# Optimization experiments

Hardware: AMD Instinct MI355X
Metric: run time of the kernel (lower is better)

## Reference

```python
import jax, jax.numpy as jnp
import numpy as np

EPS = 1e-12  # torch F.normalize eps

def l2norm(x, axis=-1):
    n = jnp.linalg.norm(x, axis=axis, keepdims=True)
    return x / jnp.maximum(n, EPS)

def setup_inputs() -> dict:
    key = jax.random.key(0)
    ks = jax.random.split(key, 8)
    n_vocab, d, n_asp = 100000, 256, 14
    B, L, M = 512, 100, 10
    pos = jax.random.randint(ks[0], (B, L), 0, n_vocab)
    negs = jax.random.randint(ks[1], (B, M, L), 0, n_vocab)
    E_w = jax.random.normal(ks[2], (n_vocab, d), dtype=jnp.float32) * 0.1
    T_w = jax.random.normal(ks[3], (n_asp, d), dtype=jnp.float32) * 0.1
    M_w = jax.random.uniform(ks[4], (d, d), dtype=jnp.float32, minval=-0.1, maxval=0.1)
    M_b = jnp.zeros((d,), dtype=jnp.float32)
    lin_w = jax.random.normal(ks[5], (n_asp, d), dtype=jnp.float32) * 0.05
    lin_b = jnp.zeros((n_asp,), dtype=jnp.float32)
    return {"pos": pos, "negs": negs, "E_w": E_w, "T_w": T_w,
            "M_w": M_w, "M_b": M_b, "lin_w": lin_w, "lin_b": lin_b}

def reference(pos, negs, E_w, T_w, M_w, M_b, lin_w, lin_b):
    # e: [B, L, d] (original keeps e_i as [B, d, L]; layout differs, math identical)
    e = E_w[pos]
    y_s = jnp.mean(e, axis=1)                    # mean over tokens -> [B, d]
    My = y_s @ M_w.T + M_b                       # [B, d]
    d_i = jnp.tanh(jnp.einsum('bld,bd->bl', e, My))  # [B, L]
    # NOTE: original normalizes exp(d_i) by the GLOBAL sum over the whole batch
    a_i = jnp.exp(d_i) / jnp.sum(jnp.exp(d_i))   # [B, L]
    z_s = l2norm(jnp.einsum('bld,bl->bd', e, a_i))   # [B, d]
    p_t = jax.nn.softmax(z_s @ lin_w.T + lin_b, axis=1)  # [B, n_asp]
    r_s = l2norm(p_t @ T_w)                      # [B, d]
    e_n = E_w[negs]                              # [B, M, L, d]
    z_n = l2norm(jnp.mean(e_n, axis=2))          # [B, M, d]
    return (r_s, z_s, z_n)
```

## Files before the change

kernel.cpp:

```cpp
#include <hip/hip_runtime.h>
#include <math.h>

#define D 256
#define LMAX 100

__device__ __forceinline__ float wave_reduce_sum(float v) {
#pragma unroll
    for (int off = 32; off > 0; off >>= 1) v += __shfl_xor(v, off);
    return v;
}

__global__ __launch_bounds__(512) void abae_main_kernel(
    const int* __restrict__ pos, const float* __restrict__ E_w,
    const float* __restrict__ T_w, const float* __restrict__ M_w,
    const float* __restrict__ M_b, const float* __restrict__ lin_w,
    const float* __restrict__ lin_b, float* __restrict__ r_s,
    float* __restrict__ z_s, int L, int n_asp) {
    const int b    = blockIdx.x;
    const int t    = threadIdx.x;
    const int lane = t & 63;
    const int wv   = t >> 6;
    const int NW   = 8;
    const int* __restrict__ posb = pos + (size_t)b * L;

    __shared__ float  se[LMAX * D];
    __shared__ float  sy[D];
    __shared__ float  smy[D];
    __shared__ float4 sred[8][64];
    __shared__ float  slog[16];
    __shared__ float  sp[16];
    __shared__ float  sscal[8];

    const int C  = (L + NW - 1) / NW;
    const int s0 = wv * C;
    const int e0 = min(L, s0 + C);

    float4 acc = make_float4(0.f, 0.f, 0.f, 0.f);
    int l = s0;
    for (; l + 3 < e0; l += 4) {
        const int i0 = posb[l], i1 = posb[l + 1], i2 = posb[l + 2], i3 = posb[l + 3];
        const float4 a0 = ((const float4*)(E_w + (size_t)i0 * D))[lane];
        const float4 a1 = ((const float4*)(E_w + (size_t)i1 * D))[lane];
        const float4 a2 = ((const float4*)(E_w + (size_t)i2 * D))[lane];
        const float4 a3 = ((const float4*)(E_w + (size_t)i3 * D))[lane];
        ((float4*)se)[(l + 0) * 64 + lane] = a0;
        ((float4*)se)[(l + 1) * 64 + lane] = a1;
        ((float4*)se)[(l + 2) * 64 + lane] = a2;
        ((float4*)se)[(l + 3) * 64 + lane] = a3;
        acc.x += a0.x + a1.x + a2.x + a3.x;
        acc.y += a0.y + a1.y + a2.y + a3.y;
        acc.z += a0.z + a1.z + a2.z + a3.z;
        acc.w += a0.w + a1.w + a2.w + a3.w;
    }
    for (; l < e0; ++l) {
        const int idx = posb[l];
        const float4 a0 = ((const float4*)(E_w + (size_t)idx * D))[lane];
        ((float4*)se)[l * 64 + lane] = a0;
        acc.x += a0.x; acc.y += a0.y; acc.z += a0.z; acc.w += a0.w;
    }
    sred[wv][lane] = acc;
    __syncthreads();
    if (wv == 0) {
        float4 y = sred[0][lane];
#pragma unroll
        for (int w = 1; w < 8; ++w) {
            const float4 a = sred[w][lane];
            y.x += a.x; y.y += a.y; y.z += a.z; y.w += a.w;
        }
        const float invL = 1.f / (float)L;
        y.x *= invL; y.y *= invL; y.z *= invL; y.w *= invL;
        ((float4*)sy)[lane] = y;
    }
    __syncthreads();

    if (t < D) {
        float m = M_b[t];
        const float4* __restrict__ mwrow = (const float4*)(M_w + (size_t)t * D);
#pragma unroll 8
        for (int k = 0; k < D / 4; ++k) {
            const float4 v = mwrow[k];
            m += sy[4 * k + 0] * v.x + sy[4 * k + 1] * v.y +
                 sy[4 * k + 2] * v.z + sy[4 * k + 3] * v.w;
        }
        smy[t] = m;
    }
    __syncthreads();

    const float4 my4 = ((const float4*)smy)[lane];
    float4 zacc = make_float4(0.f, 0.f, 0.f, 0.f);
    l = s0;
    for (; l + 1 < e0; l += 2) {
        const float4 ea = ((const float4*)se)[(l + 0) * 64 + lane];
        const float4 eb = ((const float4*)se)[(l + 1) * 64 + lane];
        float pa = ea.x * my4.x + ea.y * my4.y + ea.z * my4.z + ea.w * my4.w;
        float pb = eb.x * my4.x + eb.y * my4.y + eb.z * my4.z + eb.w * my4.w;
#pragma unroll
        for (int off = 32; off > 0; off >>= 1) {
            pa += __shfl_xor(pa, off);
            pb += __shfl_xor(pb, off);
        }
        const float wa = expf(tanhf(pa));
        const float wb = expf(tanhf(pb));
        zacc.x += ea.x * wa + eb.x * wb;
        zacc.y += ea.y * wa + eb.y * wb;
        zacc.z += ea.z * wa + eb.z * wb;
        zacc.w += ea.w * wa + eb.w * wb;
    }
    for (; l < e0; ++l) {
        const float4 ea = ((const float4*)se)[l * 64 + lane];
        float pa = ea.x * my4.x + ea.y * my4.y + ea.z * my4.z + ea.w * my4.w;
        pa = wave_reduce_sum(pa);
        const float wa = expf(tanhf(pa));
        zacc.x += ea.x * wa; zacc.y += ea.y * wa;
        zacc.z += ea.z * wa; zacc.w += ea.w * wa;
    }
    sred[wv][lane] = zacc;
    __syncthreads();
    if (wv == 0) {
        float4 z = sred[0][lane];
#pragma unroll
        for (int w = 1; w < 8; ++w) {
            const float4 a = sred[w][lane];
            z.x += a.x; z.y += a.y; z.z += a.z; z.w += a.w;
        }
        float ss = z.x * z.x + z.y * z.y + z.z * z.z + z.w * z.w;
        ss = wave_reduce_sum(ss);
        const float inv = 1.f / fmaxf(sqrtf(ss), 1e-12f);
        z.x *= inv; z.y *= inv; z.z *= inv; z.w *= inv;
        ((float4*)(z_s + (size_t)b * D))[lane] = z;
        ((float4*)sy)[lane] = z;
    }
    __syncthreads();

    const float4 z4 = ((const float4*)sy)[lane];
    for (int a = wv; a < n_asp; a += NW) {
        const float4 w4 = ((const float4*)(lin_w + (size_t)a * D))[lane];
        float p = z4.x * w4.x + z4.y * w4.y + z4.z * w4.z + z4.w * w4.w;
        p = wave_reduce_sum(p);
        if (lane == 0) slog[a] = p + lin_b[a];
    }
    __syncthreads();
    if (t == 0) {
        float mx = -1e30f;
        for (int a = 0; a < n_asp; ++a) mx = fmaxf(mx, slog[a]);
        float s = 0.f;
        for (int a = 0; a < n_asp; ++a) {
            const float e = expf(slog[a] - mx);
            sp[a] = e; s += e;
        }
        const float invs = 1.f / s;
        for (int a = 0; a < n_asp; ++a) sp[a] *= invs;
    }
    __syncthreads();

    float r = 0.f;
    if (t < D) {
        for (int a = 0; a < n_asp; ++a) r += sp[a] * T_w[(size_t)a * D + t];
    }
    float sq = wave_reduce_sum(r * r);
    if (lane == 0) sscal[wv] = sq;
    __syncthreads();
    if (t < D) {
        const float tot = sscal[0] + sscal[1] + sscal[2] + sscal[3];
        const float inv = 1.f / fmaxf(sqrtf(tot), 1e-12f);
        r_s[(size_t)b * D + t] = r * inv;
    }
}

__global__ __launch_bounds__(256) void abae_negs_kernel(
    const int* __restrict__ negs, const float* __restrict__ E_w,
    float* __restrict__ z_n, int L) {
    const int bm   = blockIdx.x;
    const int t    = threadIdx.x;
    const int lane = t & 63;
    const int wv   = t >> 6;
    const int* __restrict__ idxp = negs + (size_t)bm * L;

    const int C  = (L + 3) / 4;
    const int s0 = wv * C;
    const int e0 = min(L, s0 + C);

    float4 acc = make_float4(0.f, 0.f, 0.f, 0.f);
    int l = s0;
    for (; l + 5 <= e0; l += 5) {
        const int i0 = idxp[l], i1 = idxp[l + 1], i2 = idxp[l + 2],
                  i3 = idxp[l + 3], i4 = idxp[l + 4];
        const float4 v0 = ((const float4*)(E_w + (size_t)i0 * D))[lane];
        const float4 v1 = ((const float4*)(E_w + (size_t)i1 * D))[lane];
        const float4 v2 = ((const float4*)(E_w + (size_t)i2 * D))[lane];
        const float4 v3 = ((const float4*)(E_w + (size_t)i3 * D))[lane];
        const float4 v4 = ((const float4*)(E_w + (size_t)i4 * D))[lane];
        acc.x += v0.x + v1.x + v2.x + v3.x + v4.x;
        acc.y += v0.y + v1.y + v2.y + v3.y + v4.y;
        acc.z += v0.z + v1.z + v2.z + v3.z + v4.z;
        acc.w += v0.w + v1.w + v2.w + v3.w + v4.w;
    }
    for (; l < e0; ++l) {
        const int idx = idxp[l];
        const float4 v = ((const float4*)(E_w + (size_t)idx * D))[lane];
        acc.x += v.x; acc.y += v.y; acc.z += v.z; acc.w += v.w;
    }

    __shared__ float4 sred[4][64];
    sred[wv][lane] = acc;
    __syncthreads();
    if (wv == 0) {
        float4 z  = sred[0][lane];
        const float4 a1 = sred[1][lane], a2 = sred[2][lane], a3 = sred[3][lane];
        const float invL = 1.f / (float)L;
        z.x = (z.x + a1.x + a2.x + a3.x) * invL;
        z.y = (z.y + a1.y + a2.y + a3.y) * invL;
        z.z = (z.z + a1.z + a2.z + a3.z) * invL;
        z.w = (z.w + a1.w + a2.w + a3.w) * invL;
        float ss = z.x * z.x + z.y * z.y + z.z * z.z + z.w * z.w;
        ss = wave_reduce_sum(ss);
        const float inv = 1.f / fmaxf(sqrtf(ss), 1e-12f);
        z.x *= inv; z.y *= inv; z.z *= inv; z.w *= inv;
        ((float4*)(z_n + (size_t)bm * D))[lane] = z;
    }
}

extern "C" void kernel_launch(void* const* d_in, const int* in_sizes, int n_in,
                              void* d_out, int out_size, void* d_ws, size_t ws_size,
                              hipStream_t stream) {
    const int*   pos   = (const int*)d_in[0];
    const int*   negs  = (const int*)d_in[1];
    const float* E_w   = (const float*)d_in[2];
    const float* T_w   = (const float*)d_in[3];
    const float* M_w   = (const float*)d_in[4];
    const float* M_b   = (const float*)d_in[5];
    const float* lin_w = (const float*)d_in[6];
    const float* lin_b = (const float*)d_in[7];
    float* out = (float*)d_out;

    const int d     = in_sizes[5];
    const int n_asp = in_sizes[7];
    const int M     = in_sizes[1] / in_sizes[0];
    const int B     = out_size / (d * (2 + M));
    const int L     = in_sizes[0] / B;
    (void)d; (void)n_in; (void)d_ws; (void)ws_size;

    float* r_s = out;
    float* z_s = out + (size_t)B * d;
    float* z_n = out + (size_t)2 * B * d;

    abae_negs_kernel<<<B * M, 256, 0, stream>>>(negs, E_w, z_n, L);
    abae_main_kernel<<<B, 512, 0, stream>>>(pos, E_w, T_w, M_w, M_b, lin_w,
                                            lin_b, r_s, z_s, L, n_asp);
}
```

Before: 253.0 us.

## Fuse pos and negs kernels into one launch; drop shared-memory embedding cache

Merges the positive-path and negative-sample kernels into a single 256-thread launch. The first B blocks do the attention path and the rest do the negative means. The 100 KB shared-memory tile of gathered embeddings is removed, and the second pass re-gathers rows from E_w (likely cache hits), which should raise occupancy and let the two workloads overlap. The M_w matvec becomes coalesced row-per-wave dot products with shuffle reductions instead of one strided row per thread. The cost is a second global gather of the positive embeddings and four waves instead of eight on the main path.

Measured after the change: 228.0 us. 1.11x faster.

```diff
diff --git a/kernel.cpp b/kernel.cpp
--- a/kernel.cpp
+++ b/kernel.cpp
@@ -2,7 +2,6 @@
 #include <math.h>
 
 #define D 256
-#define LMAX 100
 
 __device__ __forceinline__ float wave_reduce_sum(float v) {
 #pragma unroll
@@ -10,79 +9,131 @@
     return v;
 }
 
-__global__ __launch_bounds__(512) void abae_main_kernel(
-    const int* __restrict__ pos, const float* __restrict__ E_w,
-    const float* __restrict__ T_w, const float* __restrict__ M_w,
-    const float* __restrict__ M_b, const float* __restrict__ lin_w,
-    const float* __restrict__ lin_b, float* __restrict__ r_s,
-    float* __restrict__ z_s, int L, int n_asp) {
-    const int b    = blockIdx.x;
+__global__ __launch_bounds__(256) void abae_fused_kernel(
+    const int* __restrict__ pos, const int* __restrict__ negs,
+    const float* __restrict__ E_w, const float* __restrict__ T_w,
+    const float* __restrict__ M_w, const float* __restrict__ M_b,
+    const float* __restrict__ lin_w, const float* __restrict__ lin_b,
+    float* __restrict__ r_s, float* __restrict__ z_s, float* __restrict__ z_n,
+    int B, int L, int n_asp) {
     const int t    = threadIdx.x;
     const int lane = t & 63;
     const int wv   = t >> 6;
-    const int NW   = 8;
-    const int* __restrict__ posb = pos + (size_t)b * L;
-
-    __shared__ float  se[LMAX * D];
+
+    __shared__ float4 sred[4][64];
     __shared__ float  sy[D];
     __shared__ float  smy[D];
-    __shared__ float4 sred[8][64];
     __shared__ float  slog[16];
     __shared__ float  sp[16];
-    __shared__ float  sscal[8];
-
-    const int C  = (L + NW - 1) / NW;
+    __shared__ float  sscal[4];
+
+    if (blockIdx.x >= B) {
+        const int bm = blockIdx.x - B;
+        const int* __restrict__ idxp = negs + (size_t)bm * L;
+        const int C  = (L + 3) / 4;
+        const int s0 = wv * C;
+        const int e0 = min(L, s0 + C);
+
+        float4 acc = make_float4(0.f, 0.f, 0.f, 0.f);
+        int l = s0;
+        for (; l + 5 <= e0; l += 5) {
+            const int i0 = idxp[l], i1 = idxp[l + 1], i2 = idxp[l + 2],
+                      i3 = idxp[l + 3], i4 = idxp[l + 4];
+            const float4 v0 = ((const float4*)(E_w + (size_t)i0 * D))[lane];
+            const float4 v1 = ((const float4*)(E_w + (size_t)i1 * D))[lane];
+            const float4 v2 = ((const float4*)(E_w + (size_t)i2 * D))[lane];
+            const float4 v3 = ((const float4*)(E_w + (size_t)i3 * D))[lane];
+            const float4 v4 = ((const float4*)(E_w + (size_t)i4 * D))[lane];
+            acc.x += v0.x + v1.x + v2.x + v3.x + v4.x;
+            acc.y += v0.y + v1.y + v2.y + v3.y + v4.y;
+            acc.z += v0.z + v1.z + v2.z + v3.z + v4.z;
+            acc.w += v0.w + v1.w + v2.w + v3.w + v4.w;
+        }
+        for (; l < e0; ++l) {
+            const float4 v = ((const float4*)(E_w + (size_t)idxp[l] * D))[lane];
+            acc.x += v.x; acc.y += v.y; acc.z += v.z; acc.w += v.w;
+        }
+        sred[wv][lane] = acc;
+        __syncthreads();
+        if (wv == 0) {
+            float4 z  = sred[0][lane];
+            const float4 a1 = sred[1][lane], a2 = sred[2][lane], a3 = sred[3][lane];
+            const float invL = 1.f / (float)L;
+            z.x = (z.x + a1.x + a2.x + a3.x) * invL;
+            z.y = (z.y + a1.y + a2.y + a3.y) * invL;
+            z.z = (z.z + a1.z + a2.z + a3.z) * invL;
+            z.w = (z.w + a1.w + a2.w + a3.w) * invL;
+            float ss = z.x * z.x + z.y * z.y + z.z * z.z + z.w * z.w;
+            ss = wave_reduce_sum(ss);
+            const float inv = 1.f / fmaxf(sqrtf(ss), 1e-12f);
+            z.x *= inv; z.y *= inv; z.z *= inv; z.w *= inv;
+            ((float4*)(z_n + (size_t)bm * D))[lane] = z;
+        }
+        return;
+    }
+
+    const int b = blockIdx.x;
+    const int* __restrict__ posb = pos + (size_t)b * L;
+    const int C  = (L + 3) / 4;
     const int s0 = wv * C;
     const int e0 = min(L, s0 + C);
 
     float4 acc = make_float4(0.f, 0.f, 0.f, 0.f);
     int l = s0;
-    for (; l + 3 < e0; l += 4) {
+    for (; l + 4 <= e0; l += 4) {
         const int i0 = posb[l], i1 = posb[l + 1], i2 = posb[l + 2], i3 = posb[l + 3];
-        const float4 a0 = ((const float4*)(E_w + (size_t)i0 * D))[lane];
-        const float4 a1 = ((const float4*)(E_w + (size_t)i1 * D))[lane];
-        const float4 a2 = ((const float4*)(E_w + (size_t)i2 * D))[lane];
-        const float4 a3 = ((const float4*)(E_w + (size_t)i3 * D))[lane];
-        ((float4*)se)[(l + 0) * 64 + lane] = a0;
-        ((float4*)se)[(l + 1) * 64 + lane] = a1;
-        ((float4*)se)[(l + 2) * 64 + lane] = a2;
-        ((float4*)se)[(l + 3) * 64 + lane] = a3;
-        acc.x += a0.x + a1.x + a2.x + a3.x;
-        acc.y += a0.y + a1.y + a2.y + a3.y;
-        acc.z += a0.z + a1.z + a2.z + a3.z;
-        acc.w += a0.w + a1.w + a2.w + a3.w;
+        const float4 v0 = ((const float4*)(E_w + (size_t)i0 * D))[lane];
+        const float4 v1 = ((const float4*)(E_w + (size_t)i1 * D))[lane];
+        const float4 v2 = ((const float4*)(E_w + (size_t)i2 * D))[lane];
+        const float4 v3 = ((const float4*)(E_w + (size_t)i3 * D))[lane];
+        acc.x += v0.x + v1.x + v2.x + v3.x;
+        acc.y += v0.y + v1.y + v2.y + v3.y;
+        acc.z += v0.z + v1.z + v2.z + v3.z;
+        acc.w += v0.w + v1.w + v2.w + v3.w;
     }
     for (; l < e0; ++l) {
-        const int idx = posb[l];
-        const float4 a0 = ((const float4*)(E_w + (size_t)idx * D))[lane];
-        ((float4*)se)[l * 64 + lane] = a0;
-        acc.x += a0.x; acc.y += a0.y; acc.z += a0.z; acc.w += a0.w;
+        const float4 v = ((const float4*)(E_w + (size_t)posb[l] * D))[lane];
+        acc.x += v.x; acc.y += v.y; acc.z += v.z; acc.w += v.w;
     }
     sred[wv][lane] = acc;
     __syncthreads();
     if (wv == 0) {
-        float4 y = sred[0][lane];
+        float4 y  = sred[0][lane];
+        const float4 a1 = sred[1][lane], a2 = sred[2][lane], a3 = sred[3][lane];
+        const float invL = 1.f / (float)L;
+        y.x = (y.x + a1.x + a2.x + a3.x) * invL;
+        y.y = (y.y + a1.y + a2.y + a3.y) * invL;
+        y.z = (y.z + a1.z + a2.z + a3.z) * invL;
+        y.w = (y.w + a1.w + a2.w + a3.w) * invL;
+        ((float4*)sy)[lane] = y;
+    }
+    __syncthreads();
+
+    {
+        const float4 y4 = ((const float4*)sy)[lane];
+        for (int r0 = wv * 64; r0 < wv * 64 + 64; r0 += 4) {
+            const float4 m0 = ((const float4*)(M_w + (size_t)(r0 + 0) * D))[lane];
+            const float4 m1 = ((const float4*)(M_w + (size_t)(r0 + 1) * D))[lane];
+            const float4 m2 = ((const float4*)(M_w + (size_t)(r0 + 2) * D))[lane];
+            const float4 m3 = ((const float4*)(M_w + (size_t)(r0 + 3) * D))[lane];
+            float p0 = m0.x * y4.x + m0.y * y4.y + m0.z * y4.z + m0.w * y4.w;
+            float p1 = m1.x * y4.x + m1.y * y4.y + m1.z * y4.z + m1.w * y4.w;
+            float p2 = m2.x * y4.x + m2.y * y4.y + m2.z * y4.z + m2.w * y4.w;
+            float p3 = m3.x * y4.x + m3.y * y4.y + m3.z * y4.z + m3.w * y4.w;
 #pragma unroll
-        for (int w = 1; w < 8; ++w) {
-            const float4 a = sred[w][lane];
-            y.x += a.x; y.y += a.y; y.z += a.z; y.w += a.w;
-        }
-        const float invL = 1.f / (float)L;
-        y.x *= invL; y.y *= invL; y.z *= invL; y.w *= invL;
-        ((float4*)sy)[lane] = y;
-    }
-    __syncthreads();
-
-    if (t < D) {
-        float m = M_b[t];
-        const float4* __restrict__ mwrow = (const float4*)(M_w + (size_t)t * D);
-#pragma unroll 8
-        for (int k = 0; k < D / 4; ++k) {
-            const float4 v = mwrow[k];
-            m += sy[4 * k + 0] * v.x + sy[4 * k + 1] * v.y +
-                 sy[4 * k + 2] * v.z + sy[4 * k + 3] * v.w;
-        }
-        smy[t] = m;
+            for (int off = 32; off > 0; off >>= 1) {
+                p0 += __shfl_xor(p0, off);
+                p1 += __shfl_xor(p1, off);
+                p2 += __shfl_xor(p2, off);
+                p3 += __shfl_xor(p3, off);
+            }
+            if (lane == 0) {
+                smy[r0 + 0] = p0 + M_b[r0 + 0];
+                smy[r0 + 1] = p1 + M_b[r0 + 1];
+                smy[r0 + 2] = p2 + M_b[r0 + 2];
+                smy[r0 + 3] = p3 + M_b[r0 + 3];
+            }
+        }
     }
     __syncthreads();
 
@@ -90,8 +141,8 @@
     float4 zacc = make_float4(0.f, 0.f, 0.f, 0.f);
     l = s0;
     for (; l + 1 < e0; l += 2) {
-        const float4 ea = ((const float4*)se)[(l + 0) * 64 + lane];
-        const float4 eb = ((const float4*)se)[(l + 1) * 64 + lane];
+        const float4 ea = ((const float4*)(E_w + (size_t)posb[l] * D))[lane];
+        const float4 eb = ((const float4*)(E_w + (size_t)posb[l + 1] * D))[lane];
         float pa = ea.x * my4.x + ea.y * my4.y + ea.z * my4.z + ea.w * my4.w;
         float pb = eb.x * my4.x + eb.y * my4.y + eb.z * my4.z + eb.w * my4.w;
 #pragma unroll
@@ -107,7 +158,7 @@
         zacc.w += ea.w * wa + eb.w * wb;
     }
     for (; l < e0; ++l) {
-        const float4 ea = ((const float4*)se)[l * 64 + lane];
+        const float4 ea = ((const float4*)(E_w + (size_t)posb[l] * D))[lane];
         float pa = ea.x * my4.x + ea.y * my4.y + ea.z * my4.z + ea.w * my4.w;
         pa = wave_reduce_sum(pa);
         const float wa = expf(tanhf(pa));
@@ -117,12 +168,12 @@
     sred[wv][lane] = zacc;
     __syncthreads();
     if (wv == 0) {
-        float4 z = sred[0][lane];
-#pragma unroll
-        for (int w = 1; w < 8; ++w) {
-            const float4 a = sred[w][lane];
-            z.x += a.x; z.y += a.y; z.z += a.z; z.w += a.w;
-        }
+        float4 z  = sred[0][lane];
+        const float4 a1 = sred[1][lane], a2 = sred[2][lane], a3 = sred[3][lane];
+        z.x += a1.x + a2.x + a3.x;
+        z.y += a1.y + a2.y + a3.y;
+        z.z += a1.z + a2.z + a3.z;
+        z.w += a1.w + a2.w + a3.w;
         float ss = z.x * z.x + z.y * z.y + z.z * z.z + z.w * z.w;
         ss = wave_reduce_sum(ss);
         const float inv = 1.f / fmaxf(sqrtf(ss), 1e-12f);
@@ -133,7 +184,7 @@
     __syncthreads();
 
     const float4 z4 = ((const float4*)sy)[lane];
-    for (int a = wv; a < n_asp; a += NW) {
+    for (int a = wv; a < n_asp; a += 4) {
         const float4 w4 = ((const float4*)(lin_w + (size_t)a * D))[lane];
         float p = z4.x * w4.x + z4.y * w4.y + z4.z * w4.z + z4.w * w4.w;
         p = wave_reduce_sum(p);
@@ -154,70 +205,13 @@
     __syncthreads();
 
     float r = 0.f;
-    if (t < D) {
-        for (int a = 0; a < n_asp; ++a) r += sp[a] * T_w[(size_t)a * D + t];
-    }
-    float sq = wave_reduce_sum(r * r);
+    for (int a = 0; a < n_asp; ++a) r += sp[a] * T_w[(size_t)a * D + t];
+    const float sq = wave_reduce_sum(r * r);
     if (lane == 0) sscal[wv] = sq;
     __syncthreads();
-    if (t < D) {
-        const float tot = sscal[0] + sscal[1] + sscal[2] + sscal[3];
-        const float inv = 1.f / fmaxf(sqrtf(tot), 1e-12f);
-        r_s[(size_t)b * D + t] = r * inv;
-    }
-}
-
-__global__ __launch_bounds__(256) void abae_negs_kernel(
-    const int* __restrict__ negs, const float* __restrict__ E_w,
-    float* __restrict__ z_n, int L) {
-    const int bm   = blockIdx.x;
-    const int t    = threadIdx.x;
-    const int lane = t & 63;
-    const int wv   = t >> 6;
-    const int* __restrict__ idxp = negs + (size_t)bm * L;
-
-    const int C  = (L + 3) / 4;
-    const int s0 = wv * C;
-    const int e0 = min(L, s0 + C);
-
-    float4 acc = make_float4(0.f, 0.f, 0.f, 0.f);
-    int l = s0;
-    for (; l + 5 <= e0; l += 5) {
-        const int i0 = idxp[l], i1 = idxp[l + 1], i2 = idxp[l + 2],
-                  i3 = idxp[l + 3], i4 = idxp[l + 4];
-        const float4 v0 = ((const float4*)(E_w + (size_t)i0 * D))[lane];
-        const float4 v1 = ((const float4*)(E_w + (size_t)i1 * D))[lane];
-        const float4 v2 = ((const float4*)(E_w + (size_t)i2 * D))[lane];
-        const float4 v3 = ((const float4*)(E_w + (size_t)i3 * D))[lane];
-        const float4 v4 = ((const float4*)(E_w + (size_t)i4 * D))[lane];
-        acc.x += v0.x + v1.x + v2.x + v3.x + v4.x;
-        acc.y += v0.y + v1.y + v2.y + v3.y + v4.y;
-        acc.z += v0.z + v1.z + v2.z + v3.z + v4.z;
-        acc.w += v0.w + v1.w + v2.w + v3.w + v4.w;
-    }
-    for (; l < e0; ++l) {
-        const int idx = idxp[l];
-        const float4 v = ((const float4*)(E_w + (size_t)idx * D))[lane];
-        acc.x += v.x; acc.y += v.y; acc.z += v.z; acc.w += v.w;
-    }
-
-    __shared__ float4 sred[4][64];
-    sred[wv][lane] = acc;
-    __syncthreads();
-    if (wv == 0) {
-        float4 z  = sred[0][lane];
-        const float4 a1 = sred[1][lane], a2 = sred[2][lane], a3 = sred[3][lane];
-        const float invL = 1.f / (float)L;
-        z.x = (z.x + a1.x + a2.x + a3.x) * invL;
-        z.y = (z.y + a1.y + a2.y + a3.y) * invL;
-        z.z = (z.z + a1.z + a2.z + a3.z) * invL;
-        z.w = (z.w + a1.w + a2.w + a3.w) * invL;
-        float ss = z.x * z.x + z.y * z.y + z.z * z.z + z.w * z.w;
-        ss = wave_reduce_sum(ss);
-        const float inv = 1.f / fmaxf(sqrtf(ss), 1e-12f);
-        z.x *= inv; z.y *= inv; z.z *= inv; z.w *= inv;
-        ((float4*)(z_n + (size_t)bm * D))[lane] = z;
-    }
+    const float tot = sscal[0] + sscal[1] + sscal[2] + sscal[3];
+    const float inv = 1.f / fmaxf(sqrtf(tot), 1e-12f);
+    r_s[(size_t)b * D + t] = r * inv;
 }
 
 extern "C" void kernel_launch(void* const* d_in, const int* in_sizes, int n_in,
@@ -244,7 +238,6 @@
     float* z_s = out + (size_t)B * d;
     float* z_n = out + (size_t)2 * B * d;
 
-    abae_negs_kernel<<<B * M, 256, 0, stream>>>(negs, E_w, z_n, L);
-    abae_main_kernel<<<B, 512, 0, stream>>>(pos, E_w, T_w, M_w, M_b, lin_w,
-                                            lin_b, r_s, z_s, L, n_asp);
+    abae_fused_kernel<<<B + B * M, 256, 0, stream>>>(
+        pos, negs, E_w, T_w, M_w, M_b, lin_w, lin_b, r_s, z_s, z_n, B, L, n_asp);
 }
```
